# Optimization experiments

Hardware: AMD Instinct MI355X
Metric: run time of the kernel (lower is better)

## Reference

```python
import jax, jax.numpy as jnp
import numpy as np

B, L, C, H, W = 2, 3, 64, 32, 32
DI, N, DT_RANK, K = 128, 16, 4, 4  # d_inner=2*C, d_state, dt_rank=ceil(C/16), 4 scan dirs


def setup_inputs() -> dict:
    key = jax.random.key(0)
    ks = iter(jax.random.split(key, 48))
    nrm = lambda shape, s=0.02: jax.random.normal(next(ks), shape, jnp.float32) * s
    return {
        "image_sequence": jax.random.normal(next(ks), (B, L, C, H, W), jnp.float32),
        "difficult_zone": jax.random.normal(next(ks), (B, C, H, W), jnp.float32),
        "sigma": jax.random.uniform(next(ks), (B, C, H, W), jnp.float32),
        # LayerNorm2d applied to each frame
        "norm_g": jnp.ones((C,)), "norm_b": jnp.zeros((C,)),
        # ConvolutionalResBlock (in=3C -> out=C), GroupNorm(num_groups=1)
        "gn1_g": jnp.ones((3 * C,)), "gn1_b": jnp.zeros((3 * C,)),
        "conv1_w": nrm((C, 3 * C, 3, 3)), "conv1_b": jnp.zeros((C,)),
        "gn2_g": jnp.ones((C,)), "gn2_b": jnp.zeros((C,)),
        "conv2_w": nrm((C, C, 3, 3)), "conv2_b": jnp.zeros((C,)),
        "skip_w": nrm((C, 3 * C, 1, 1)), "skip_b": jnp.zeros((C,)),
        # VSSBlock pre-norms
        "ln1_g": jnp.ones((C,)), "ln1_b": jnp.zeros((C,)),
        "ln2_g": jnp.ones((C,)), "ln2_b": jnp.zeros((C,)),
        # SS2D
        "in_proj_w": nrm((2 * DI, C)),
        "dwconv_w": nrm((DI, 1, 3, 3)), "dwconv_b": jnp.zeros((DI,)),
        "x_proj_w": nrm((K, DT_RANK + 2 * N, DI)),
        "dt_proj_w": nrm((K, DI, DT_RANK), 0.1),
        "dt_proj_b": jnp.log(jnp.expm1(jnp.full((K, DI), 0.01, jnp.float32))),
        "A_logs": jnp.log(jnp.tile(jnp.arange(1, N + 1, dtype=jnp.float32), (K * DI, 1))),
        "Ds": jnp.ones((K * DI,)),
        "out_norm_g": jnp.ones((DI,)), "out_norm_b": jnp.zeros((DI,)),
        "out_proj_w": nrm((C, DI)),
        # Mlp (hidden = C)
        "fc1_w": nrm((C, C)), "fc1_b": jnp.zeros((C,)),
        "fc2_w": nrm((C, C)), "fc2_b": jnp.zeros((C,)),
    }


def _ln(x, g, b, eps=1e-5):  # layernorm over last axis
    m = x.mean(-1, keepdims=True)
    v = x.var(-1, keepdims=True)
    return (x - m) * jax.lax.rsqrt(v + eps) * g + b


def _ln2d(x, g, b, eps=1e-6):  # per-pixel channel layernorm, NCHW
    m = x.mean(1, keepdims=True)
    v = x.var(1, keepdims=True)
    return (x - m) * jax.lax.rsqrt(v + eps) * g[None, :, None, None] + b[None, :, None, None]


def _gn1(x, g, b, eps=1e-5):  # GroupNorm(num_groups=1), NCHW
    m = x.mean((1, 2, 3), keepdims=True)
    v = x.var((1, 2, 3), keepdims=True)
    return (x - m) * jax.lax.rsqrt(v + eps) * g[None, :, None, None] + b[None, :, None, None]


def _conv(x, w, b, pad):
    y = jax.lax.conv_general_dilated(x, w, (1, 1), [(pad, pad), (pad, pad)],
                                     dimension_numbers=("NCHW", "OIHW", "NCHW"))
    return y + b[None, :, None, None]


def _forward(image_sequence, difficult_zone, sigma, norm_g, norm_b, gn1_g, gn1_b,
             conv1_w, conv1_b, gn2_g, gn2_b, conv2_w, conv2_b, skip_w, skip_b,
             ln1_g, ln1_b, ln2_g, ln2_b, in_proj_w, dwconv_w, dwconv_b, x_proj_w,
             dt_proj_w, dt_proj_b, A_logs, Ds, out_norm_g, out_norm_b, out_proj_w,
             fc1_w, fc1_b, fc2_w, fc2_b):
    b, l, c, h, w = image_sequence.shape
    bl, L2 = b * l, h * w
    # fold frame loop into batch (identical math per frame in the torch loop)
    frames = _ln2d(image_sequence.reshape(bl, c, h, w), norm_g, norm_b)
    dz = jnp.broadcast_to(difficult_zone[:, None], (b, l, c, h, w)).reshape(bl, c, h, w)
    sg = jnp.broadcast_to(sigma[:, None], (b, l, c, h, w)).reshape(bl, c, h, w)
    x = jnp.concatenate([dz, frames, sg], axis=1)  # [bl, 3c, h, w]
    # channel compressor: pre-act conv res block
    hdn = _conv(jax.nn.silu(_gn1(x, gn1_g, gn1_b)), conv1_w, conv1_b, 1)
    hdn = _conv(jax.nn.silu(_gn1(hdn, gn2_g, gn2_b)), conv2_w, conv2_b, 1)
    x = hdn + _conv(x, skip_w, skip_b, 0)          # [bl, c, h, w]
    x = x.transpose(0, 2, 3, 1)                    # [bl, h, w, c]
    # --- VSSBlock (pre-norm): x = x + SS2D(LN(x)) ---
    xn = _ln(x, ln1_g, ln1_b)
    xz = xn @ in_proj_w.T                          # [bl,h,w,2*DI]
    xc, z = jnp.split(xz, 2, axis=-1)
    xc = xc.transpose(0, 3, 1, 2)                  # [bl, DI, h, w]
    xc = jax.lax.conv_general_dilated(xc, dwconv_w, (1, 1), [(1, 1), (1, 1)],
                                      dimension_numbers=("NCHW", "OIHW", "NCHW"),
                                      feature_group_count=DI) + dwconv_b[None, :, None, None]
    xc = jax.nn.silu(xc)
    # 4-direction scan inputs (HW, WH, and their reverses)
    xf = xc.reshape(bl, DI, L2)
    xt = xc.transpose(0, 1, 3, 2).reshape(bl, DI, L2)
    xs = jnp.stack([xf, xt], axis=1)
    xs = jnp.concatenate([xs, jnp.flip(xs, axis=-1)], axis=1)  # [bl, 4, DI, L2]
    x_dbl = jnp.einsum("bkdl,kcd->bkcl", xs, x_proj_w)
    dts, Bs, Cs = jnp.split(x_dbl, [DT_RANK, DT_RANK + N], axis=2)
    dts = jnp.einsum("bkrl,kdr->bkdl", dts, dt_proj_w) + dt_proj_b[None, :, :, None]
    dts = jax.nn.softplus(dts)                     # [bl, 4, DI, L2]
    A = -jnp.exp(A_logs).reshape(K, DI, N)
    dA = jnp.exp(dts[..., None] * A[None, :, :, None, :])            # [bl,4,DI,L2,N]
    dBu = dts[..., None] * Bs.transpose(0, 1, 3, 2)[:, :, None] * xs[..., None]
    a_t = dA.transpose(3, 0, 1, 2, 4)              # [L2, bl, 4, DI, N]
    bu_t = dBu.transpose(3, 0, 1, 2, 4)
    c_t = Cs.transpose(3, 0, 1, 2)                 # [L2, bl, 4, N]

    def step(hid, inp):
        a_i, bu_i, c_i = inp
        hid = a_i * hid + bu_i
        return hid, jnp.einsum("bkdn,bkn->bkd", hid, c_i)

    h0 = jnp.zeros((bl, K, DI, N), xs.dtype)
    _, ys = jax.lax.scan(step, h0, (a_t, bu_t, c_t))                 # [L2, bl, 4, DI]
    ys = ys.transpose(1, 2, 3, 0) + xs * Ds.reshape(K, DI)[None, :, :, None]
    inv = jnp.flip(ys[:, 2:4], axis=-1)
    y = (ys[:, 0] + inv[:, 0]
         + ys[:, 1].reshape(bl, DI, w, h).transpose(0, 1, 3, 2).reshape(bl, DI, L2)
         + inv[:, 1].reshape(bl, DI, w, h).transpose(0, 1, 3, 2).reshape(bl, DI, L2))
    y = _ln(y.transpose(0, 2, 1), out_norm_g, out_norm_b).reshape(bl, h, w, DI)
    y = y * jax.nn.silu(z)
    x = x + y @ out_proj_w.T
    # --- x = x + Mlp(LN(x)) ---
    xn = _ln(x, ln2_g, ln2_b)
    x = x + (jax.nn.gelu(xn @ fc1_w.T + fc1_b, approximate=False) @ fc2_w.T + fc2_b)
    return x.transpose(0, 3, 1, 2).reshape(b, l, c, h, w)


def reference(image_sequence, difficult_zone, sigma, norm_g, norm_b, gn1_g, gn1_b,
              conv1_w, conv1_b, gn2_g, gn2_b, conv2_w, conv2_b, skip_w, skip_b,
              ln1_g, ln1_b, ln2_g, ln2_b, in_proj_w, dwconv_w, dwconv_b, x_proj_w,
              dt_proj_w, dt_proj_b, A_logs, Ds, out_norm_g, out_norm_b, out_proj_w,
              fc1_w, fc1_b, fc2_w, fc2_b):
    return _forward(image_sequence, difficult_zone, sigma, norm_g, norm_b, gn1_g, gn1_b,
                    conv1_w, conv1_b, gn2_g, gn2_b, conv2_w, conv2_b, skip_w, skip_b,
                    ln1_g, ln1_b, ln2_g, ln2_b, in_proj_w, dwconv_w, dwconv_b, x_proj_w,
                    dt_proj_w, dt_proj_b, A_logs, Ds, out_norm_g, out_norm_b, out_proj_w,
                    fc1_w, fc1_b, fc2_w, fc2_b)
```

## Files before the change

kernel.cpp:

```cpp
#include <hip/hip_runtime.h>
#include <math.h>

#define BL    6
#define CCH   64
#define C3    192
#define L2    1024
#define DIC   128
#define NST   16
#define K4    4
#define PSTR  1088
#define NCH   32

#define LOG2E 1.44269504088896340736f
#define LN2C  0.69314718055994530942f

__device__ __forceinline__ float fexp(float x){ return __builtin_amdgcn_exp2f(x*LOG2E); }
__device__ __forceinline__ float fsilu(float x){ return x * __builtin_amdgcn_rcpf(1.f + fexp(-x)); }
__device__ __forceinline__ float fsoftplus(float x){
  if (x > 20.f) return x;
  return __builtin_amdgcn_logf(1.f + fexp(x)) * LN2C;
}
__device__ __forceinline__ float fgelu(float x){
  return 0.5f*x*(1.f + erff(x*0.70710678118654752440f));
}

__global__ __launch_bounds__(256) void k_ln2d(const float* __restrict__ img,
    const float* __restrict__ dz, const float* __restrict__ sg,
    const float* __restrict__ g, const float* __restrict__ b, float* __restrict__ x3c,
    float* __restrict__ psum1, float* __restrict__ psq1){
  __shared__ float ps[4][16], pq[4][16], gs[4], gq[4];
  int s = blockIdx.x >> 6;
  int pg = blockIdx.x & 63;
  int tid = threadIdx.x;
  int px = tid & 15; int cg = tid >> 4;
  int wv = tid >> 6; int lane = tid & 63;
  int p = pg*16 + px;
  int bsmp = s/3;
  const float* fr = img + (size_t)s*CCH*L2;
  float vals[4]; float sm=0.f, sq=0.f;
  #pragma unroll
  for (int j=0;j<4;++j){
    int c = cg*4 + j;
    float v = fr[c*L2 + p];
    vals[j]=v; sm+=v; sq+=v*v;
  }
  sm += __shfl_xor(sm,16,64); sq += __shfl_xor(sq,16,64);
  sm += __shfl_xor(sm,32,64); sq += __shfl_xor(sq,32,64);
  if (lane < 16){ ps[wv][lane]=sm; pq[wv][lane]=sq; }
  __syncthreads();
  sm = ps[0][px]+ps[1][px]+ps[2][px]+ps[3][px];
  sq = pq[0][px]+pq[1][px]+pq[2][px]+pq[3][px];
  float mean = sm*(1.f/CCH); float var = sq*(1.f/CCH)-mean*mean;
  float rs = rsqrtf(var + 1e-6f);
  float* o = x3c + (size_t)s*C3*L2;
  const float* dzp = dz + (size_t)bsmp*CCH*L2;
  const float* sgp = sg + (size_t)bsmp*CCH*L2;
  float gsm=0.f, gsq=0.f;
  #pragma unroll
  for (int j=0;j<4;++j){
    int c = cg*4+j;
    float dzv = dzp[c*L2+p];
    float nv  = (vals[j]-mean)*rs*g[c] + b[c];
    float sgv = sgp[c*L2+p];
    o[c*L2+p] = dzv;
    o[(CCH+c)*L2+p] = nv;
    o[(2*CCH+c)*L2+p] = sgv;
    gsm += dzv+nv+sgv; gsq += dzv*dzv+nv*nv+sgv*sgv;
  }
  for (int m=1;m<64;m<<=1){ gsm+=__shfl_xor(gsm,m,64); gsq+=__shfl_xor(gsq,m,64); }
  if (lane==0){ gs[wv]=gsm; gq[wv]=gsq; }
  __syncthreads();
  if (tid==0){
    psum1[blockIdx.x] = gs[0]+gs[1]+gs[2]+gs[3];
    psq1 [blockIdx.x] = gq[0]+gq[1]+gq[2]+gq[3];
  }
}

__global__ __launch_bounds__(256) void k_gnact_pad(const float* __restrict__ x,
    const float* __restrict__ psum, const float* __restrict__ psq,
    const float* __restrict__ g, const float* __restrict__ b,
    int ch, int parts, float inv_n, float eps, float* __restrict__ out){
  int bx = blockIdx.x;
  int s = bx / ch; int c = bx % ch;
  int tid = threadIdx.x;
  float sm=0.f, sq=0.f;
  for (int i=0;i<parts;++i){ sm += psum[s*parts+i]; sq += psq[s*parts+i]; }
  float mean = sm*inv_n;
  float var = sq*inv_n - mean*mean;
  float rs = rsqrtf(var + eps);
  float gc = g[c]*rs; float bc = b[c] - mean*rs*g[c];
  float4 v = *(const float4*)(x + (size_t)bx*1024 + tid*4);
  float4 o; o.x = fsilu(v.x*gc+bc); o.y = fsilu(v.y*gc+bc);
  o.z = fsilu(v.z*gc+bc); o.w = fsilu(v.w*gc+bc);
  float* pl = out + (size_t)bx*PSTR;
  *(float4*)(pl + 32 + tid*4) = o;
  float4 z4 = make_float4(0.f,0.f,0.f,0.f);
  if (tid < 8)  *(float4*)(pl + tid*4) = z4;
  else if (tid < 16) *(float4*)(pl + 1056 + (tid-8)*4) = z4;
}

__device__ __forceinline__ void conv_row_acc(float4& a0, float4& a1, float4 mid, float lf, float rt,
    const float* wp0, const float* wp1){
  float w0=wp0[0], w1=wp0[1], w2=wp0[2];
  a0.x = fmaf(w0,lf,   fmaf(w1,mid.x, fmaf(w2,mid.y, a0.x)));
  a0.y = fmaf(w0,mid.x,fmaf(w1,mid.y, fmaf(w2,mid.z, a0.y)));
  a0.z = fmaf(w0,mid.y,fmaf(w1,mid.z, fmaf(w2,mid.w, a0.z)));
  a0.w = fmaf(w0,mid.z,fmaf(w1,mid.w, fmaf(w2,rt,    a0.w)));
  float v0=wp1[0], v1=wp1[1], v2=wp1[2];
  a1.x = fmaf(v0,lf,   fmaf(v1,mid.x, fmaf(v2,mid.y, a1.x)));
  a1.y = fmaf(v0,mid.x,fmaf(v1,mid.y, fmaf(v2,mid.z, a1.y)));
  a1.z = fmaf(v0,mid.y,fmaf(v1,mid.z, fmaf(v2,mid.w, a1.z)));
  a1.w = fmaf(v0,mid.z,fmaf(v1,mid.w, fmaf(v2,rt,    a1.w)));
}

__device__ __forceinline__ void conv_ci_body(float4 m0, float4 m1, float4 m2, int q,
    const float* wp0, const float* wp1, float4& a0, float4& a1){
  float lf0=__shfl_up(m0.w,1,64), rt0=__shfl_down(m0.x,1,64);
  float lf1=__shfl_up(m1.w,1,64), rt1=__shfl_down(m1.x,1,64);
  float lf2=__shfl_up(m2.w,1,64), rt2=__shfl_down(m2.x,1,64);
  if (q==0){ lf0=0.f; lf1=0.f; lf2=0.f; }
  if (q==7){ rt0=0.f; rt1=0.f; rt2=0.f; }
  conv_row_acc(a0,a1,m0,lf0,rt0, wp0+0, wp1+0);
  conv_row_acc(a0,a1,m1,lf1,rt1, wp0+3, wp1+3);
  conv_row_acc(a0,a1,m2,lf2,rt2, wp0+6, wp1+6);
}

__global__ __launch_bounds__(256) void k_conv1_split(const float* __restrict__ xact,
    const float* __restrict__ w, float* __restrict__ part){
  int bx = blockIdx.x; int kk = bx&7; int cop=(bx>>3)&31; int s=bx>>8;
  int co0 = cop*2, co1 = co0+1;
  int tid = threadIdx.x; int row = tid>>3; int q = tid&7; int col0 = q*4;
  float4 a0 = make_float4(0.f,0.f,0.f,0.f);
  float4 a1 = make_float4(0.f,0.f,0.f,0.f);
  int ci0 = kk*24;
  const float* pl = xact + ((size_t)s*C3 + ci0)*PSTR + row*32 + col0;
  const float* wp0 = w + (size_t)(co0*C3 + ci0)*9;
  const float* wp1 = w + (size_t)(co1*C3 + ci0)*9;
  float4 m0 = *(const float4*)(pl);
  float4 m1 = *(const float4*)(pl+32);
  float4 m2 = *(const float4*)(pl+64);
  #pragma unroll 2
  for (int i=0;i<24;++i){
    const float* pn = pl + (i<23 ? PSTR : 0);
    float4 n0 = *(const float4*)(pn);
    float4 n1 = *(const float4*)(pn+32);
    float4 n2 = *(const float4*)(pn+64);
    conv_ci_body(m0,m1,m2,q, wp0, wp1, a0, a1);
    wp0 += 9; wp1 += 9; pl = pn; m0=n0; m1=n1; m2=n2;
  }
  float* pp = part + (size_t)kk*(BL*CCH*L2) + ((size_t)s*CCH+co0)*L2 + row*32+col0;
  *(float4*)pp = a0;
  *(float4*)(pp+L2) = a1;
}

__global__ __launch_bounds__(256) void k_reduce1(const float* __restrict__ part,
    const float* __restrict__ bias, float* __restrict__ h1,
    float* __restrict__ psum2, float* __restrict__ psq2){
  int co = blockIdx.x & 63; int s = blockIdx.x >> 6;
  size_t ofs = ((size_t)s*CCH+co)*L2 + threadIdx.x*4;
  const size_t stride = (size_t)BL*CCH*L2;
  float4 acc = *(const float4*)(part + ofs);
  #pragma unroll
  for (int kk=1;kk<8;++kk){
    float4 r = *(const float4*)(part + (size_t)kk*stride + ofs);
    acc.x += r.x; acc.y += r.y; acc.z += r.z; acc.w += r.w;
  }
  float bv = bias[co];
  acc.x += bv; acc.y += bv; acc.z += bv; acc.w += bv;
  *(float4*)(h1 + ofs) = acc;
  float sm = acc.x+acc.y+acc.z+acc.w;
  float sq = acc.x*acc.x+acc.y*acc.y+acc.z*acc.z+acc.w*acc.w;
  for (int m=1;m<64;m<<=1){ sm+=__shfl_xor(sm,m,64); sq+=__shfl_xor(sq,m,64); }
  __shared__ float s_sm[4], s_sq[4];
  int wv = threadIdx.x>>6;
  if ((threadIdx.x&63)==0){ s_sm[wv]=sm; s_sq[wv]=sq; }
  __syncthreads();
  if (threadIdx.x==0){
    psum2[blockIdx.x] = s_sm[0]+s_sm[1]+s_sm[2]+s_sm[3];
    psq2 [blockIdx.x] = s_sq[0]+s_sq[1]+s_sq[2]+s_sq[3];
  }
}

__global__ __launch_bounds__(256) void k_conv2_split(const float* __restrict__ xact2,
    const float* __restrict__ x3c, const float* __restrict__ w2,
    const float* __restrict__ wsk, float* __restrict__ part){
  int t = blockIdx.x; int role = t % 3; t /= 3;
  int cop = t & 31; int s = t >> 5;
  int co0 = cop*2, co1 = co0+1;
  int tid = threadIdx.x; int row = tid>>3; int q = tid&7; int col0 = q*4;
  int p = row*32+col0;
  float4 a0 = make_float4(0.f,0.f,0.f,0.f);
  float4 a1 = make_float4(0.f,0.f,0.f,0.f);
  if (role < 2){
    int ci0 = role*32;
    const float* pl = xact2 + ((size_t)s*CCH + ci0)*PSTR + row*32 + col0;
    const float* wp0 = w2 + (size_t)(co0*CCH + ci0)*9;
    const float* wp1 = w2 + (size_t)(co1*CCH + ci0)*9;
    float4 m0 = *(const float4*)(pl);
    float4 m1 = *(const float4*)(pl+32);
    float4 m2 = *(const float4*)(pl+64);
    #pragma unroll 2
    for (int i=0;i<32;++i){
      const float* pn = pl + (i<31 ? PSTR : 0);
      float4 n0 = *(const float4*)(pn);
      float4 n1 = *(const float4*)(pn+32);
      float4 n2 = *(const float4*)(pn+64);
      conv_ci_body(m0,m1,m2,q, wp0, wp1, a0, a1);
      wp0 += 9; wp1 += 9; pl = pn; m0=n0; m1=n1; m2=n2;
    }
  } else {
    const float* x3 = x3c + (size_t)s*C3*L2 + p;
    #pragma unroll 4
    for (int ci=0; ci<C3; ++ci){
      float4 v = *(const float4*)(x3 + (size_t)ci*L2);
      float ws0 = wsk[co0*C3+ci], ws1 = wsk[co1*C3+ci];
      a0.x = fmaf(ws0,v.x,a0.x); a0.y = fmaf(ws0,v.y,a0.y); a0.z = fmaf(ws0,v.z,a0.z); a0.w = fmaf(ws0,v.w,a0.w);
      a1.x = fmaf(ws1,v.x,a1.x); a1.y = fmaf(ws1,v.y,a1.y); a1.z = fmaf(ws1,v.z,a1.z); a1.w = fmaf(ws1,v.w,a1.w);
    }
  }
  float* pp = part + (size_t)role*(BL*CCH*L2) + ((size_t)s*CCH+co0)*L2 + p;
  *(float4*)pp = a0;
  *(float4*)(pp+L2) = a1;
}

__global__ __launch_bounds__(256) void k_red2_ln1_inproj(const float* __restrict__ part,
    const float* __restrict__ b2, const float* __restrict__ bsk,
    const float* __restrict__ g, const float* __restrict__ b,
    const float* __restrict__ W,
    float* __restrict__ x_cmaj, float* __restrict__ xc, float* __restrict__ z_t){
  __shared__ float xn_s[64*65];
  int bx = blockIdx.x; int oq = bx & 3; int pg = (bx>>2)&15; int s = bx>>6;
  int p0 = pg*64;
  int tid = threadIdx.x;
  const size_t stride = (size_t)BL*CCH*L2;
  #pragma unroll
  for (int kq=0;kq<4;++kq){
    int f = kq*256 + tid;
    int co = f >> 4; int px4 = (f & 15)*4;
    size_t ofs = ((size_t)s*CCH+co)*L2 + p0 + px4;
    float4 r0 = *(const float4*)(part + ofs);
    float4 r1 = *(const float4*)(part + stride + ofs);
    float4 r2 = *(const float4*)(part + 2*stride + ofs);
    float bv = b2[co]+bsk[co];
    float4 o;
    o.x = r0.x+r1.x+r2.x+bv;
    o.y = r0.y+r1.y+r2.y+bv;
    o.z = r0.z+r1.z+r2.z+bv;
    o.w = r0.w+r1.w+r2.w+bv;
    if (oq == 0) *(float4*)(x_cmaj + ofs) = o;
    xn_s[(px4+0)*65 + co] = o.x;
    xn_s[(px4+1)*65 + co] = o.y;
    xn_s[(px4+2)*65 + co] = o.z;
    xn_s[(px4+3)*65 + co] = o.w;
  }
  __syncthreads();
  {
    int wv = __builtin_amdgcn_readfirstlane(tid>>6); int lane = tid&63;
    for (int j=0;j<16;++j){
      int pl = wv*16 + j;
      float v = xn_s[pl*65 + lane];
      float sm = v, sq = v*v;
      for (int m=1;m<64;m<<=1){ sm += __shfl_xor(sm,m,64); sq += __shfl_xor(sq,m,64); }
      float mean = sm*(1.f/64.f); float var = sq*(1.f/64.f) - mean*mean;
      float rs = rsqrtf(var + 1e-5f);
      xn_s[pl*65 + lane] = (v-mean)*rs*g[lane] + b[lane];
    }
  }
  __syncthreads();
  int px_l = tid & 63;
  int og = __builtin_amdgcn_readfirstlane(tid >> 6);
  int o0 = oq*64 + og*16;
  float acc[16];
  #pragma unroll
  for (int oi=0;oi<16;++oi) acc[oi]=0.f;
  for (int c=0;c<64;++c){
    float xv = xn_s[px_l*65 + c];
    #pragma unroll
    for (int oi=0;oi<16;++oi) acc[oi] = fmaf(W[(o0+oi)*64 + c], xv, acc[oi]);
  }
  int p = p0 + px_l;
  if (oq < 2){
    #pragma unroll
    for (int oi=0;oi<16;++oi) xc[((size_t)s*DIC + o0 + oi)*L2 + p] = acc[oi];
  } else {
    #pragma unroll
    for (int oi=0;oi<16;++oi) z_t[((size_t)s*DIC + (o0-128) + oi)*L2 + p] = acc[oi];
  }
}

__global__ __launch_bounds__(256) void k_xproj_dt(const float* __restrict__ xc,
    const float* __restrict__ dww, const float* __restrict__ dwb,
    const float* __restrict__ W,
    float* __restrict__ dtr, float* __restrict__ Bp, float* __restrict__ Cp,
    float* __restrict__ u_t){
  __shared__ float smem[128*68];
  int bx = blockIdx.x; int pg = bx & 15; int sk = bx >> 4;
  int k = sk & 3; int s = sk >> 2;
  int tid = threadIdx.x;
  for (int i = tid; i < 128*16; i += 256){
    int dr = i>>4; int j4 = (i&15)*4;
    int rw = j4>>5; int col0 = j4 & 31;
    int gr = pg*2 + rw;
    int q = i&7;
    const float* xr = xc + ((size_t)s*DIC+dr)*L2;
    const float* wp = dww + dr*9;
    float bv = dwb[dr];
    float4 acc = make_float4(bv,bv,bv,bv);
    #pragma unroll
    for (int dy=-1;dy<=1;++dy){
      int r = gr+dy;
      float4 mid = make_float4(0.f,0.f,0.f,0.f);
      if (0<=r && r<32) mid = *(const float4*)(xr + r*32 + col0);
      float lf = __shfl_up(mid.w,1,64); if(q==0) lf=0.f;
      float rt = __shfl_down(mid.x,1,64); if(q==7) rt=0.f;
      float w0=wp[(dy+1)*3], w1=wp[(dy+1)*3+1], w2=wp[(dy+1)*3+2];
      acc.x = fmaf(w0,lf,   fmaf(w1,mid.x, fmaf(w2,mid.y, acc.x)));
      acc.y = fmaf(w0,mid.x,fmaf(w1,mid.y, fmaf(w2,mid.z, acc.y)));
      acc.z = fmaf(w0,mid.y,fmaf(w1,mid.z, fmaf(w2,mid.w, acc.z)));
      acc.w = fmaf(w0,mid.z,fmaf(w1,mid.w, fmaf(w2,rt,    acc.w)));
    }
    acc.x = fsilu(acc.x); acc.y = fsilu(acc.y); acc.z = fsilu(acc.z); acc.w = fsilu(acc.w);
    *(float4*)&smem[dr*68 + j4] = acc;
  }
  __syncthreads();
  if (k == 0){
    float* ub = u_t + ((size_t)(s*L2) + pg*64)*DIC;
    for (int i = tid; i < 64*128; i += 256){
      int px2 = i>>7; int dd = i&127;
      ub[(size_t)px2*DIC + dd] = smem[dd*68 + px2];
    }
  }
  int px = tid & 63;
  int cgrp = __builtin_amdgcn_readfirstlane(tid >> 6);
  int c0 = cgrp*9;
  const float* wb = W + (size_t)(k*36 + c0)*DIC;
  float acc[9];
  #pragma unroll
  for (int ci=0;ci<9;++ci) acc[ci]=0.f;
  for (int d=0; d<DIC; ++d){
    float xv = smem[d*68 + px];
    #pragma unroll
    for (int ci=0;ci<9;++ci) acc[ci] = fmaf(wb[ci*DIC+d], xv, acc[ci]);
  }
  __syncthreads();
  #pragma unroll
  for (int ci=0;ci<9;++ci) smem[(c0+ci)*68 + px] = acc[ci];
  __syncthreads();
  {
    int pp = tid >> 2; int r = tid & 3;
    dtr[((size_t)sk*L2 + pg*64 + pp)*4 + r] = smem[r*68 + pp];
  }
  float* Bb = Bp + ((size_t)sk*L2 + pg*64)*NST;
  float* Cb = Cp + ((size_t)sk*L2 + pg*64)*NST;
  for (int i = tid; i < 1024; i += 256){
    int pp = i>>4; int n = i&15;
    Bb[pp*NST + n] = smem[(4+n)*68 + pp];
    Cb[pp*NST + n] = smem[(20+n)*68 + pp];
  }
}

__device__ __forceinline__ int scan_pix32(int ch, int j, int k){
  if (k==0) return ch*32 + j;
  if (k==1) return j*32 + ch;
  if (k==2) return 1023 - (ch*32 + j);
  return 1023 - (j*32 + ch);
}

struct StepB { float4 dt4; float uv; float4 B0,B1,B2,B3; };
__device__ __forceinline__ StepB loadB(const float* dr, const float* ub, const float* Bb, int p){
  StepB r;
  r.dt4 = *(const float4*)(dr + (size_t)p*4);
  r.uv = ub[(size_t)p*DIC];
  const float* bp = Bb + p*NST;
  r.B0 = *(const float4*)bp; r.B1 = *(const float4*)(bp+4);
  r.B2 = *(const float4*)(bp+8); r.B3 = *(const float4*)(bp+12);
  return r;
}
__device__ __forceinline__ float dt_eval(float4 w4, float bb, float4 d4){
  return fsoftplus(fmaf(w4.x,d4.x,fmaf(w4.y,d4.y,fmaf(w4.z,d4.z,fmaf(w4.w,d4.w,bb)))));
}

__global__ __launch_bounds__(256,2) void k_scan_part3(const float* __restrict__ dtr,
    const float* __restrict__ dtw, const float* __restrict__ dtb,
    const float* __restrict__ u_t, const float* __restrict__ Bp,
    const float* __restrict__ A_logs, float* __restrict__ hend, float* __restrict__ Ssum){
  int bx = blockIdx.x; int chp = bx & 15; int sk = bx >> 4;
  int k = sk & 3; int s = sk >> 2;
  int tid = threadIdx.x; int d = tid & 127; int ch = chp*2 + (tid>>7);
  float aco[16];
  {
    const float* ab = A_logs + (size_t)(k*DIC+d)*NST;
    #pragma unroll
    for (int n=0;n<16;++n) aco[n] = -LOG2E * fexp(ab[n]);
  }
  float4 w4 = *(const float4*)(dtw + (size_t)(k*DIC+d)*4);
  float bb = dtb[k*DIC+d];
  float h[16]; float Sacc = 0.f;
  #pragma unroll
  for (int n=0;n<16;++n) h[n]=0.f;
  const float* dr = dtr + (size_t)sk*L2*4;
  const float* ub = u_t + (size_t)s*L2*DIC + d;
  const float* Bb = Bp + (size_t)sk*L2*NST;
  StepB cur = loadB(dr, ub, Bb, scan_pix32(ch, 0, k));
  #pragma unroll 4
  for (int j=0;j<32;++j){
    StepB nxt;
    if (j < 31) nxt = loadB(dr, ub, Bb, scan_pix32(ch, j+1, k));
    float dtv = dt_eval(w4, bb, cur.dt4);
    Sacc += dtv;
    float tv = dtv*cur.uv;
    #define PSTEP(NI, BV) { float a_ = __builtin_amdgcn_exp2f(dtv*aco[NI]); \
      h[NI] = fmaf(a_, h[NI], tv*(BV)); }
    PSTEP(0,cur.B0.x) PSTEP(1,cur.B0.y) PSTEP(2,cur.B0.z) PSTEP(3,cur.B0.w)
    PSTEP(4,cur.B1.x) PSTEP(5,cur.B1.y) PSTEP(6,cur.B1.z) PSTEP(7,cur.B1.w)
    PSTEP(8,cur.B2.x) PSTEP(9,cur.B2.y) PSTEP(10,cur.B2.z) PSTEP(11,cur.B2.w)
    PSTEP(12,cur.B3.x) PSTEP(13,cur.B3.y) PSTEP(14,cur.B3.z) PSTEP(15,cur.B3.w)
    #undef PSTEP
    cur = nxt;
  }
  size_t base = ((size_t)(sk*NCH + ch)*DIC + d)*NST;
  #pragma unroll
  for (int q4=0;q4<4;++q4)
    *(float4*)(hend + base + q4*4)  = make_float4(h[q4*4],h[q4*4+1],h[q4*4+2],h[q4*4+3]);
  Ssum[(size_t)(sk*NCH + ch)*DIC + d] = Sacc;
}

__global__ __launch_bounds__(256) void k_scan_fix3(const float* __restrict__ hend,
    const float* __restrict__ Ssum, const float* __restrict__ A_logs,
    float* __restrict__ Hin){
  int t = blockIdx.x*256 + threadIdx.x;
  int n = t & 15; int d = (t>>4) & 127; int sk = t >> 11; int k = sk & 3;
  float aco = -LOG2E * fexp(A_logs[(size_t)(k*DIC+d)*NST + n]);
  float H = 0.f;
  #pragma unroll 8
  for (int ch=0; ch<NCH; ++ch){
    size_t sidx = (size_t)(sk*NCH + ch)*DIC + d;
    float pa = __builtin_amdgcn_exp2f(aco * Ssum[sidx]);
    float he = hend[sidx*NST + n];
    Hin[sidx*NST + n] = H;
    H = fmaf(pa, H, he);
  }
}

__global__ __launch_bounds__(256,2) void k_scan_y3(const float* __restrict__ dtr,
    const float* __restrict__ dtw, const float* __restrict__ dtb,
    const float* __restrict__ u_t, const float* __restrict__ Bp, const float* __restrict__ Cp,
    const float* __restrict__ A_logs, const float* __restrict__ Ds,
    const float* __restrict__ Hin, float* __restrict__ ys_t){
  int bx = blockIdx.x; int chp = bx & 15; int sk = bx >> 4;
  int k = sk & 3; int s = sk >> 2;
  int tid = threadIdx.x; int d = tid & 127; int ch = chp*2 + (tid>>7);
  float aco[16];
  {
    const float* ab = A_logs + (size_t)(k*DIC+d)*NST;
    #pragma unroll
    for (int n=0;n<16;++n) aco[n] = -LOG2E * fexp(ab[n]);
  }
  float4 w4 = *(const float4*)(dtw + (size_t)(k*DIC+d)*4);
  float bb = dtb[k*DIC+d];
  float Dv = Ds[k*DIC+d];
  float h[16];
  size_t hbase = ((size_t)(sk*NCH + ch)*DIC + d)*NST;
  #pragma unroll
  for (int q4=0;q4<4;++q4){
    float4 hv = *(const float4*)(Hin + hbase + q4*4);
    h[q4*4]=hv.x; h[q4*4+1]=hv.y; h[q4*4+2]=hv.z; h[q4*4+3]=hv.w;
  }
  const float* dr = dtr + (size_t)sk*L2*4;
  const float* ub = u_t + (size_t)s*L2*DIC + d;
  const float* Bb = Bp + (size_t)sk*L2*NST;
  const float* Cb = Cp + (size_t)sk*L2*NST;
  float* yb = ys_t + (size_t)sk*L2*DIC + d;
  int pcur = scan_pix32(ch, 0, k);
  StepB cur = loadB(dr, ub, Bb, pcur);
  float4 Cc0 = *(const float4*)(Cb + pcur*NST);
  float4 Cc1 = *(const float4*)(Cb + pcur*NST + 4);
  float4 Cc2 = *(const float4*)(Cb + pcur*NST + 8);
  float4 Cc3 = *(const float4*)(Cb + pcur*NST + 12);
  #pragma unroll 4
  for (int j=0;j<32;++j){
    StepB nxt; float4 Cn0, Cn1, Cn2, Cn3; int pn = pcur;
    if (j < 31){
      pn = scan_pix32(ch, j+1, k);
      nxt = loadB(dr, ub, Bb, pn);
      Cn0 = *(const float4*)(Cb + pn*NST);
      Cn1 = *(const float4*)(Cb + pn*NST + 4);
      Cn2 = *(const float4*)(Cb + pn*NST + 8);
      Cn3 = *(const float4*)(Cb + pn*NST + 12);
    }
    float dtv = dt_eval(w4, bb, cur.dt4);
    float tv = dtv*cur.uv;
    float y0=0.f, y1=0.f, y2=0.f, y3=0.f;
    #define YSTEP(NI, BV, CV, YA) { float a_ = __builtin_amdgcn_exp2f(dtv*aco[NI]); \
      h[NI] = fmaf(a_, h[NI], tv*(BV)); YA = fmaf(h[NI], (CV), YA); }
    YSTEP(0,cur.B0.x,Cc0.x,y0) YSTEP(1,cur.B0.y,Cc0.y,y1) YSTEP(2,cur.B0.z,Cc0.z,y2) YSTEP(3,cur.B0.w,Cc0.w,y3)
    YSTEP(4,cur.B1.x,Cc1.x,y0) YSTEP(5,cur.B1.y,Cc1.y,y1) YSTEP(6,cur.B1.z,Cc1.z,y2) YSTEP(7,cur.B1.w,Cc1.w,y3)
    YSTEP(8,cur.B2.x,Cc2.x,y0) YSTEP(9,cur.B2.y,Cc2.y,y1) YSTEP(10,cur.B2.z,Cc2.z,y2) YSTEP(11,cur.B2.w,Cc2.w,y3)
    YSTEP(12,cur.B3.x,Cc3.x,y0) YSTEP(13,cur.B3.y,Cc3.y,y1) YSTEP(14,cur.B3.z,Cc3.z,y2) YSTEP(15,cur.B3.w,Cc3.w,y3)
    #undef YSTEP
    yb[(size_t)pcur*DIC] = fmaf(cur.uv, Dv, (y0+y1)+(y2+y3));
    cur = nxt; Cc0 = Cn0; Cc1 = Cn1; Cc2 = Cn2; Cc3 = Cn3; pcur = pn;
  }
}

__global__ __launch_bounds__(256) void k_tail(const float* __restrict__ ys_t,
    const float* __restrict__ z_t, const float* __restrict__ ong, const float* __restrict__ onb,
    const float* __restrict__ Wop, const float* __restrict__ x_cmaj,
    const float* __restrict__ g2, const float* __restrict__ b2n,
    const float* __restrict__ w1, const float* __restrict__ b1,
    const float* __restrict__ w2, const float* __restrict__ b2,
    float* __restrict__ out){
  __shared__ float yt[128*17];
  __shared__ float xvt[64*17];
  __shared__ float ts[64*17];
  int s = blockIdx.x >> 6; int pg = blockIdx.x & 63;
  int tid = threadIdx.x;
  {
    int wv = __builtin_amdgcn_readfirstlane(tid>>6); int lane = tid&63;
    int d0 = lane, d1 = lane+64;
    for (int i=0;i<4;++i){
      int px = i*4 + wv; int p = pg*16 + px;
      const float* yb = ys_t + ((size_t)(s*4)*L2 + p)*DIC;
      float ya = yb[d0] + yb[(size_t)L2*DIC + d0] + yb[(size_t)2*L2*DIC + d0] + yb[(size_t)3*L2*DIC + d0];
      float yc = yb[d1] + yb[(size_t)L2*DIC + d1] + yb[(size_t)2*L2*DIC + d1] + yb[(size_t)3*L2*DIC + d1];
      float sm = ya+yc, sq = ya*ya+yc*yc;
      for (int m=1;m<64;m<<=1){ sm+=__shfl_xor(sm,m,64); sq+=__shfl_xor(sq,m,64); }
      float mean = sm*(1.f/128.f); float var = sq*(1.f/128.f)-mean*mean;
      float rs = rsqrtf(var + 1e-5f);
      float yn0 = (ya-mean)*rs*ong[d0] + onb[d0];
      float yn1 = (yc-mean)*rs*ong[d1] + onb[d1];
      float zv0 = z_t[((size_t)s*DIC+d0)*L2 + p];
      float zv1 = z_t[((size_t)s*DIC+d1)*L2 + p];
      yt[d0*17 + px] = yn0 * fsilu(zv0);
      yt[d1*17 + px] = yn1 * fsilu(zv1);
    }
  }
  __syncthreads();
  {
    int px = tid & 15; int cgp = tid >> 4;
    int c0 = cgp*4;
    float a0=0.f,a1=0.f,a2=0.f,a3=0.f;
    for (int d=0; d<DIC; ++d){
      float yv = yt[d*17 + px];
      a0 = fmaf(Wop[(c0+0)*DIC + d], yv, a0);
      a1 = fmaf(Wop[(c0+1)*DIC + d], yv, a1);
      a2 = fmaf(Wop[(c0+2)*DIC + d], yv, a2);
      a3 = fmaf(Wop[(c0+3)*DIC + d], yv, a3);
    }
    int p = pg*16 + px;
    size_t base = ((size_t)s*CCH + c0)*L2 + p;
    xvt[(c0+0)*17 + px] = x_cmaj[base]      + a0;
    xvt[(c0+1)*17 + px] = x_cmaj[base+L2]   + a1;
    xvt[(c0+2)*17 + px] = x_cmaj[base+2*L2] + a2;
    xvt[(c0+3)*17 + px] = x_cmaj[base+3*L2] + a3;
  }
  __syncthreads();
  int px = tid & 15; int cgp = tid >> 4;
  float sm=0.f, sq=0.f;
  for (int c=0;c<64;++c){ float v = xvt[c*17+px]; sm+=v; sq+=v*v; }
  float mean = sm*(1.f/64.f);
  float rs = rsqrtf(sq*(1.f/64.f) - mean*mean + 1e-5f);
  int o0 = cgp*4;
  float t[4];
  #pragma unroll
  for (int oi=0;oi<4;++oi) t[oi] = b1[o0+oi];
  for (int c=0;c<64;++c){
    float xn = (xvt[c*17+px]-mean)*rs*g2[c] + b2n[c];
    #pragma unroll
    for (int oi=0;oi<4;++oi) t[oi] = fmaf(xn, w1[(o0+oi)*64 + c], t[oi]);
  }
  #pragma unroll
  for (int oi=0;oi<4;++oi) ts[(o0+oi)*17 + px] = fgelu(t[oi]);
  __syncthreads();
  int c0 = cgp*4;
  float acc[4];
  #pragma unroll
  for (int ci=0;ci<4;++ci) acc[ci] = xvt[(c0+ci)*17+px] + b2[c0+ci];
  for (int o=0;o<64;++o){
    float tv = ts[o*17+px];
    #pragma unroll
    for (int ci=0;ci<4;++ci) acc[ci] = fmaf(tv, w2[(c0+ci)*64 + o], acc[ci]);
  }
  int p = pg*16 + px;
  #pragma unroll
  for (int ci=0;ci<4;++ci) out[((size_t)s*CCH + c0+ci)*L2 + p] = acc[ci];
}

extern "C" void kernel_launch(void* const* d_in, const int* in_sizes, int n_in,
                              void* d_out, int out_size, void* d_ws, size_t ws_size,
                              hipStream_t stream){
  (void)in_sizes; (void)n_in; (void)out_size; (void)ws_size;
  const float* img      = (const float*)d_in[0];
  const float* dz       = (const float*)d_in[1];
  const float* sg       = (const float*)d_in[2];
  const float* norm_g   = (const float*)d_in[3];
  const float* norm_b   = (const float*)d_in[4];
  const float* gn1_g    = (const float*)d_in[5];
  const float* gn1_b    = (const float*)d_in[6];
  const float* conv1_w  = (const float*)d_in[7];
  const float* conv1_b  = (const float*)d_in[8];
  const float* gn2_g    = (const float*)d_in[9];
  const float* gn2_b    = (const float*)d_in[10];
  const float* conv2_w  = (const float*)d_in[11];
  const float* conv2_b  = (const float*)d_in[12];
  const float* skip_w   = (const float*)d_in[13];
  const float* skip_b   = (const float*)d_in[14];
  const float* ln1_g    = (const float*)d_in[15];
  const float* ln1_b    = (const float*)d_in[16];
  const float* ln2_g    = (const float*)d_in[17];
  const float* ln2_b    = (const float*)d_in[18];
  const float* in_proj_w= (const float*)d_in[19];
  const float* dwconv_w = (const float*)d_in[20];
  const float* dwconv_b = (const float*)d_in[21];
  const float* x_proj_w = (const float*)d_in[22];
  const float* dt_proj_w= (const float*)d_in[23];
  const float* dt_proj_b= (const float*)d_in[24];
  const float* A_logs   = (const float*)d_in[25];
  const float* Ds       = (const float*)d_in[26];
  const float* out_norm_g = (const float*)d_in[27];
  const float* out_norm_b = (const float*)d_in[28];
  const float* out_proj_w = (const float*)d_in[29];
  const float* fc1_w    = (const float*)d_in[30];
  const float* fc1_b    = (const float*)d_in[31];
  const float* fc2_w    = (const float*)d_in[32];
  const float* fc2_b    = (const float*)d_in[33];

  float* ws = (float*)d_ws;
  float* x3c    = ws;
  float* xact1  = x3c    + 1179648;
  float* h1     = xact1  + 1253376;
  float* xact2  = h1     + 393216;
  float* xpslot = xact2  + 417792;
  float* x_cmaj = xpslot + 393216;
  float* z_t    = x_cmaj + 393216;
  float* xc     = z_t    + 786432;
  float* cpslot = xc     + 786432;
  float* hole   = cpslot + 786432;
  float* scanbuf= hole   + 884736;
  float* ys_t   = scanbuf+ 3145728;
  float* statsb = ys_t   + 3145728;
  float* psum1  = statsb;
  float* psq1   = statsb + 384;
  float* psum2  = statsb + 768;
  float* psq2   = statsb + 1152;
  float* part1  = scanbuf;
  float* part2  = ys_t;
  float* hend   = x3c;
  float* u_t    = h1;
  float* Bp     = xpslot;
  float* Cp     = cpslot;
  float* dtr    = hole;
  float* Ssum   = hole + 98304;
  float* Hin    = scanbuf;

  k_ln2d<<<384, 256, 0, stream>>>(img, dz, sg, norm_g, norm_b, x3c, psum1, psq1);
  k_gnact_pad<<<6*C3, 256, 0, stream>>>(x3c, psum1, psq1, gn1_g, gn1_b, C3, 64,
                                        1.f/(C3*L2), 1e-5f, xact1);
  k_conv1_split<<<1536, 256, 0, stream>>>(xact1, conv1_w, part1);
  k_reduce1<<<384, 256, 0, stream>>>(part1, conv1_b, h1, psum2, psq2);
  k_gnact_pad<<<6*CCH, 256, 0, stream>>>(h1, psum2, psq2, gn2_g, gn2_b, CCH, 64,
                                         1.f/(CCH*L2), 1e-5f, xact2);
  k_conv2_split<<<576, 256, 0, stream>>>(xact2, x3c, conv2_w, skip_w, part2);
  k_red2_ln1_inproj<<<384, 256, 0, stream>>>(part2, conv2_b, skip_b, ln1_g, ln1_b, in_proj_w,
                                             x_cmaj, xc, z_t);
  k_xproj_dt<<<384, 256, 0, stream>>>(xc, dwconv_w, dwconv_b, x_proj_w, dtr, Bp, Cp, u_t);
  k_scan_part3<<<384, 256, 0, stream>>>(dtr, dt_proj_w, dt_proj_b, u_t, Bp, A_logs, hend, Ssum);
  k_scan_fix3<<<192, 256, 0, stream>>>(hend, Ssum, A_logs, Hin);
  k_scan_y3<<<384, 256, 0, stream>>>(dtr, dt_proj_w, dt_proj_b, u_t, Bp, Cp, A_logs, Ds, Hin, ys_t);
  k_tail<<<384, 256, 0, stream>>>(ys_t, z_t, out_norm_g, out_norm_b, out_proj_w, x_cmaj,
                                  ln2_g, ln2_b, fc1_w, fc1_b, fc2_w, fc2_b, (float*)d_out);
}
```

Baseline: 305.3 us.

## Split conv2, in_proj and scan kernels across more blocks for parallelism

Conv2 and skip work is split six ways along input channels instead of three. The reduction now sums six partials, and in_proj uses eight output groups instead of four. Both scan kernels split the 16 state dims across thread pairs, launching one chunk per block with twice the blocks and combining y via a lane shuffle. This adds CU occupancy on a small problem at the cost of more partial-buffer traffic, duplicated loads of dt and u, and a larger part2 buffer that must fit its aliased slot.

```diff
diff --git a/kernel.cpp b/kernel.cpp
--- a/kernel.cpp
+++ b/kernel.cpp
@@ -184,15 +184,15 @@
 __global__ __launch_bounds__(256) void k_conv2_split(const float* __restrict__ xact2,
     const float* __restrict__ x3c, const float* __restrict__ w2,
     const float* __restrict__ wsk, float* __restrict__ part){
-  int t = blockIdx.x; int role = t % 3; t /= 3;
+  int t = blockIdx.x; int role = t % 6; t /= 6;
   int cop = t & 31; int s = t >> 5;
   int co0 = cop*2, co1 = co0+1;
   int tid = threadIdx.x; int row = tid>>3; int q = tid&7; int col0 = q*4;
   int p = row*32+col0;
   float4 a0 = make_float4(0.f,0.f,0.f,0.f);
   float4 a1 = make_float4(0.f,0.f,0.f,0.f);
-  if (role < 2){
-    int ci0 = role*32;
+  if (role < 4){
+    int ci0 = role*16;
     const float* pl = xact2 + ((size_t)s*CCH + ci0)*PSTR + row*32 + col0;
     const float* wp0 = w2 + (size_t)(co0*CCH + ci0)*9;
     const float* wp1 = w2 + (size_t)(co1*CCH + ci0)*9;
@@ -200,8 +200,8 @@
     float4 m1 = *(const float4*)(pl+32);
     float4 m2 = *(const float4*)(pl+64);
     #pragma unroll 2
-    for (int i=0;i<32;++i){
-      const float* pn = pl + (i<31 ? PSTR : 0);
+    for (int i=0;i<16;++i){
+      const float* pn = pl + (i<15 ? PSTR : 0);
       float4 n0 = *(const float4*)(pn);
       float4 n1 = *(const float4*)(pn+32);
       float4 n2 = *(const float4*)(pn+64);
@@ -209,11 +209,14 @@
       wp0 += 9; wp1 += 9; pl = pn; m0=n0; m1=n1; m2=n2;
     }
   } else {
-    const float* x3 = x3c + (size_t)s*C3*L2 + p;
+    int ci0 = (role-4)*96;
+    const float* x3 = x3c + ((size_t)s*C3 + ci0)*L2 + p;
+    const float* w0p = wsk + co0*C3 + ci0;
+    const float* w1p = wsk + co1*C3 + ci0;
     #pragma unroll 4
-    for (int ci=0; ci<C3; ++ci){
+    for (int ci=0; ci<96; ++ci){
       float4 v = *(const float4*)(x3 + (size_t)ci*L2);
-      float ws0 = wsk[co0*C3+ci], ws1 = wsk[co1*C3+ci];
+      float ws0 = w0p[ci], ws1 = w1p[ci];
       a0.x = fmaf(ws0,v.x,a0.x); a0.y = fmaf(ws0,v.y,a0.y); a0.z = fmaf(ws0,v.z,a0.z); a0.w = fmaf(ws0,v.w,a0.w);
       a1.x = fmaf(ws1,v.x,a1.x); a1.y = fmaf(ws1,v.y,a1.y); a1.z = fmaf(ws1,v.z,a1.z); a1.w = fmaf(ws1,v.w,a1.w);
     }
@@ -229,7 +232,7 @@
     const float* __restrict__ W,
     float* __restrict__ x_cmaj, float* __restrict__ xc, float* __restrict__ z_t){
   __shared__ float xn_s[64*65];
-  int bx = blockIdx.x; int oq = bx & 3; int pg = (bx>>2)&15; int s = bx>>6;
+  int bx = blockIdx.x; int oq = bx & 7; int pg = (bx>>3)&15; int s = bx>>7;
   int p0 = pg*64;
   int tid = threadIdx.x;
   const size_t stride = (size_t)BL*CCH*L2;
@@ -241,12 +244,15 @@
     float4 r0 = *(const float4*)(part + ofs);
     float4 r1 = *(const float4*)(part + stride + ofs);
     float4 r2 = *(const float4*)(part + 2*stride + ofs);
+    float4 r3 = *(const float4*)(part + 3*stride + ofs);
+    float4 r4 = *(const float4*)(part + 4*stride + ofs);
+    float4 r5 = *(const float4*)(part + 5*stride + ofs);
     float bv = b2[co]+bsk[co];
     float4 o;
-    o.x = r0.x+r1.x+r2.x+bv;
-    o.y = r0.y+r1.y+r2.y+bv;
-    o.z = r0.z+r1.z+r2.z+bv;
-    o.w = r0.w+r1.w+r2.w+bv;
+    o.x = ((r0.x+r1.x)+(r2.x+r3.x))+(r4.x+r5.x)+bv;
+    o.y = ((r0.y+r1.y)+(r2.y+r3.y))+(r4.y+r5.y)+bv;
+    o.z = ((r0.z+r1.z)+(r2.z+r3.z))+(r4.z+r5.z)+bv;
+    o.w = ((r0.w+r1.w)+(r2.w+r3.w))+(r4.w+r5.w)+bv;
     if (oq == 0) *(float4*)(x_cmaj + ofs) = o;
     xn_s[(px4+0)*65 + co] = o.x;
     xn_s[(px4+1)*65 + co] = o.y;
@@ -269,22 +275,22 @@
   __syncthreads();
   int px_l = tid & 63;
   int og = __builtin_amdgcn_readfirstlane(tid >> 6);
-  int o0 = oq*64 + og*16;
-  float acc[16];
-  #pragma unroll
-  for (int oi=0;oi<16;++oi) acc[oi]=0.f;
+  int o0 = oq*32 + og*8;
+  float acc[8];
+  #pragma unroll
+  for (int oi=0;oi<8;++oi) acc[oi]=0.f;
   for (int c=0;c<64;++c){
     float xv = xn_s[px_l*65 + c];
     #pragma unroll
-    for (int oi=0;oi<16;++oi) acc[oi] = fmaf(W[(o0+oi)*64 + c], xv, acc[oi]);
+    for (int oi=0;oi<8;++oi) acc[oi] = fmaf(W[(o0+oi)*64 + c], xv, acc[oi]);
   }
   int p = p0 + px_l;
-  if (oq < 2){
-    #pragma unroll
-    for (int oi=0;oi<16;++oi) xc[((size_t)s*DIC + o0 + oi)*L2 + p] = acc[oi];
+  if (oq < 4){
+    #pragma unroll
+    for (int oi=0;oi<8;++oi) xc[((size_t)s*DIC + o0 + oi)*L2 + p] = acc[oi];
   } else {
     #pragma unroll
-    for (int oi=0;oi<16;++oi) z_t[((size_t)s*DIC + (o0-128) + oi)*L2 + p] = acc[oi];
+    for (int oi=0;oi<8;++oi) z_t[((size_t)s*DIC + (o0-128) + oi)*L2 + p] = acc[oi];
   }
 }
 
@@ -366,46 +372,45 @@
   return 1023 - (j*32 + ch);
 }
 
-struct StepB { float4 dt4; float uv; float4 B0,B1,B2,B3; };
-__device__ __forceinline__ StepB loadB(const float* dr, const float* ub, const float* Bb, int p){
-  StepB r;
+struct StepH { float4 dt4; float uv; float4 B0,B1; };
+__device__ __forceinline__ StepH loadH(const float* dr, const float* ub, const float* Bb, int p){
+  StepH r;
   r.dt4 = *(const float4*)(dr + (size_t)p*4);
   r.uv = ub[(size_t)p*DIC];
   const float* bp = Bb + p*NST;
   r.B0 = *(const float4*)bp; r.B1 = *(const float4*)(bp+4);
-  r.B2 = *(const float4*)(bp+8); r.B3 = *(const float4*)(bp+12);
   return r;
 }
 __device__ __forceinline__ float dt_eval(float4 w4, float bb, float4 d4){
   return fsoftplus(fmaf(w4.x,d4.x,fmaf(w4.y,d4.y,fmaf(w4.z,d4.z,fmaf(w4.w,d4.w,bb)))));
 }
 
-__global__ __launch_bounds__(256,2) void k_scan_part3(const float* __restrict__ dtr,
+__global__ __launch_bounds__(256,4) void k_scan_part3(const float* __restrict__ dtr,
     const float* __restrict__ dtw, const float* __restrict__ dtb,
     const float* __restrict__ u_t, const float* __restrict__ Bp,
     const float* __restrict__ A_logs, float* __restrict__ hend, float* __restrict__ Ssum){
-  int bx = blockIdx.x; int chp = bx & 15; int sk = bx >> 4;
+  int bx = blockIdx.x; int ch = bx & 31; int sk = bx >> 5;
   int k = sk & 3; int s = sk >> 2;
-  int tid = threadIdx.x; int d = tid & 127; int ch = chp*2 + (tid>>7);
-  float aco[16];
+  int tid = threadIdx.x; int d = tid >> 1; int nh = tid & 1;
+  float aco[8];
   {
-    const float* ab = A_logs + (size_t)(k*DIC+d)*NST;
-    #pragma unroll
-    for (int n=0;n<16;++n) aco[n] = -LOG2E * fexp(ab[n]);
+    const float* ab = A_logs + (size_t)(k*DIC+d)*NST + nh*8;
+    #pragma unroll
+    for (int n=0;n<8;++n) aco[n] = -LOG2E * fexp(ab[n]);
   }
   float4 w4 = *(const float4*)(dtw + (size_t)(k*DIC+d)*4);
   float bb = dtb[k*DIC+d];
-  float h[16]; float Sacc = 0.f;
-  #pragma unroll
-  for (int n=0;n<16;++n) h[n]=0.f;
+  float h[8]; float Sacc = 0.f;
+  #pragma unroll
+  for (int n=0;n<8;++n) h[n]=0.f;
   const float* dr = dtr + (size_t)sk*L2*4;
   const float* ub = u_t + (size_t)s*L2*DIC + d;
-  const float* Bb = Bp + (size_t)sk*L2*NST;
-  StepB cur = loadB(dr, ub, Bb, scan_pix32(ch, 0, k));
+  const float* Bb = Bp + (size_t)sk*L2*NST + nh*8;
+  StepH cur = loadH(dr, ub, Bb, scan_pix32(ch, 0, k));
   #pragma unroll 4
   for (int j=0;j<32;++j){
-    StepB nxt;
-    if (j < 31) nxt = loadB(dr, ub, Bb, scan_pix32(ch, j+1, k));
+    StepH nxt;
+    if (j < 31) nxt = loadH(dr, ub, Bb, scan_pix32(ch, j+1, k));
     float dtv = dt_eval(w4, bb, cur.dt4);
     Sacc += dtv;
     float tv = dtv*cur.uv;
@@ -413,16 +418,13 @@
       h[NI] = fmaf(a_, h[NI], tv*(BV)); }
     PSTEP(0,cur.B0.x) PSTEP(1,cur.B0.y) PSTEP(2,cur.B0.z) PSTEP(3,cur.B0.w)
     PSTEP(4,cur.B1.x) PSTEP(5,cur.B1.y) PSTEP(6,cur.B1.z) PSTEP(7,cur.B1.w)
-    PSTEP(8,cur.B2.x) PSTEP(9,cur.B2.y) PSTEP(10,cur.B2.z) PSTEP(11,cur.B2.w)
-    PSTEP(12,cur.B3.x) PSTEP(13,cur.B3.y) PSTEP(14,cur.B3.z) PSTEP(15,cur.B3.w)
     #undef PSTEP
     cur = nxt;
   }
-  size_t base = ((size_t)(sk*NCH + ch)*DIC + d)*NST;
-  #pragma unroll
-  for (int q4=0;q4<4;++q4)
-    *(float4*)(hend + base + q4*4)  = make_float4(h[q4*4],h[q4*4+1],h[q4*4+2],h[q4*4+3]);
-  Ssum[(size_t)(sk*NCH + ch)*DIC + d] = Sacc;
+  size_t base = ((size_t)(sk*NCH + ch)*DIC + d)*NST + nh*8;
+  *(float4*)(hend + base)     = make_float4(h[0],h[1],h[2],h[3]);
+  *(float4*)(hend + base + 4) = make_float4(h[4],h[5],h[6],h[7]);
+  if (nh == 0) Ssum[(size_t)(sk*NCH + ch)*DIC + d] = Sacc;
 }
 
 __global__ __launch_bounds__(256) void k_scan_fix3(const float* __restrict__ hend,
@@ -442,51 +444,48 @@
   }
 }
 
-__global__ __launch_bounds__(256,2) void k_scan_y3(const float* __restrict__ dtr,
+__global__ __launch_bounds__(256,4) void k_scan_y3(const float* __restrict__ dtr,
     const float* __restrict__ dtw, const float* __restrict__ dtb,
     const float* __restrict__ u_t, const float* __restrict__ Bp, const float* __restrict__ Cp,
     const float* __restrict__ A_logs, const float* __restrict__ Ds,
     const float* __restrict__ Hin, float* __restrict__ ys_t){
-  int bx = blockIdx.x; int chp = bx & 15; int sk = bx >> 4;
+  int bx = blockIdx.x; int ch = bx & 31; int sk = bx >> 5;
   int k = sk & 3; int s = sk >> 2;
-  int tid = threadIdx.x; int d = tid & 127; int ch = chp*2 + (tid>>7);
-  float aco[16];
+  int tid = threadIdx.x; int d = tid >> 1; int nh = tid & 1;
+  float aco[8];
   {
-    const float* ab = A_logs + (size_t)(k*DIC+d)*NST;
-    #pragma unroll
-    for (int n=0;n<16;++n) aco[n] = -LOG2E * fexp(ab[n]);
+    const float* ab = A_logs + (size_t)(k*DIC+d)*NST + nh*8;
+    #pragma unroll
+    for (int n=0;n<8;++n) aco[n] = -LOG2E * fexp(ab[n]);
   }
   float4 w4 = *(const float4*)(dtw + (size_t)(k*DIC+d)*4);
   float bb = dtb[k*DIC+d];
   float Dv = Ds[k*DIC+d];
-  float h[16];
-  size_t hbase = ((size_t)(sk*NCH + ch)*DIC + d)*NST;
-  #pragma unroll
-  for (int q4=0;q4<4;++q4){
-    float4 hv = *(const float4*)(Hin + hbase + q4*4);
-    h[q4*4]=hv.x; h[q4*4+1]=hv.y; h[q4*4+2]=hv.z; h[q4*4+3]=hv.w;
+  float h[8];
+  size_t hbase = ((size_t)(sk*NCH + ch)*DIC + d)*NST + nh*8;
+  {
+    float4 h0 = *(const float4*)(Hin + hbase);
+    float4 h1 = *(const float4*)(Hin + hbase + 4);
+    h[0]=h0.x; h[1]=h0.y; h[2]=h0.z; h[3]=h0.w;
+    h[4]=h1.x; h[5]=h1.y; h[6]=h1.z; h[7]=h1.w;
   }
   const float* dr = dtr + (size_t)sk*L2*4;
   const float* ub = u_t + (size_t)s*L2*DIC + d;
-  const float* Bb = Bp + (size_t)sk*L2*NST;
-  const float* Cb = Cp + (size_t)sk*L2*NST;
+  const float* Bb = Bp + (size_t)sk*L2*NST + nh*8;
+  const float* Cb = Cp + (size_t)sk*L2*NST + nh*8;
   float* yb = ys_t + (size_t)sk*L2*DIC + d;
   int pcur = scan_pix32(ch, 0, k);
-  StepB cur = loadB(dr, ub, Bb, pcur);
+  StepH cur = loadH(dr, ub, Bb, pcur);
   float4 Cc0 = *(const float4*)(Cb + pcur*NST);
   float4 Cc1 = *(const float4*)(Cb + pcur*NST + 4);
-  float4 Cc2 = *(const float4*)(Cb + pcur*NST + 8);
-  float4 Cc3 = *(const float4*)(Cb + pcur*NST + 12);
   #pragma unroll 4
   for (int j=0;j<32;++j){
-    StepB nxt; float4 Cn0, Cn1, Cn2, Cn3; int pn = pcur;
+    StepH nxt; float4 Cn0, Cn1; int pn = pcur;
     if (j < 31){
       pn = scan_pix32(ch, j+1, k);
-      nxt = loadB(dr, ub, Bb, pn);
+      nxt = loadH(dr, ub, Bb, pn);
       Cn0 = *(const float4*)(Cb + pn*NST);
       Cn1 = *(const float4*)(Cb + pn*NST + 4);
-      Cn2 = *(const float4*)(Cb + pn*NST + 8);
-      Cn3 = *(const float4*)(Cb + pn*NST + 12);
     }
     float dtv = dt_eval(w4, bb, cur.dt4);
     float tv = dtv*cur.uv;
@@ -495,11 +494,11 @@
       h[NI] = fmaf(a_, h[NI], tv*(BV)); YA = fmaf(h[NI], (CV), YA); }
     YSTEP(0,cur.B0.x,Cc0.x,y0) YSTEP(1,cur.B0.y,Cc0.y,y1) YSTEP(2,cur.B0.z,Cc0.z,y2) YSTEP(3,cur.B0.w,Cc0.w,y3)
     YSTEP(4,cur.B1.x,Cc1.x,y0) YSTEP(5,cur.B1.y,Cc1.y,y1) YSTEP(6,cur.B1.z,Cc1.z,y2) YSTEP(7,cur.B1.w,Cc1.w,y3)
-    YSTEP(8,cur.B2.x,Cc2.x,y0) YSTEP(9,cur.B2.y,Cc2.y,y1) YSTEP(10,cur.B2.z,Cc2.z,y2) YSTEP(11,cur.B2.w,Cc2.w,y3)
-    YSTEP(12,cur.B3.x,Cc3.x,y0) YSTEP(13,cur.B3.y,Cc3.y,y1) YSTEP(14,cur.B3.z,Cc3.z,y2) YSTEP(15,cur.B3.w,Cc3.w,y3)
     #undef YSTEP
-    yb[(size_t)pcur*DIC] = fmaf(cur.uv, Dv, (y0+y1)+(y2+y3));
-    cur = nxt; Cc0 = Cn0; Cc1 = Cn1; Cc2 = Cn2; Cc3 = Cn3; pcur = pn;
+    float py = (y0+y1)+(y2+y3);
+    float tot = py + __shfl_xor(py, 1, 64);
+    if (nh == 0) yb[(size_t)pcur*DIC] = fmaf(cur.uv, Dv, tot);
+    cur = nxt; Cc0 = Cn0; Cc1 = Cn1; pcur = pn;
   }
 }
 
@@ -660,13 +659,13 @@
   k_reduce1<<<384, 256, 0, stream>>>(part1, conv1_b, h1, psum2, psq2);
   k_gnact_pad<<<6*CCH, 256, 0, stream>>>(h1, psum2, psq2, gn2_g, gn2_b, CCH, 64,
                                          1.f/(CCH*L2), 1e-5f, xact2);
-  k_conv2_split<<<576, 256, 0, stream>>>(xact2, x3c, conv2_w, skip_w, part2);
-  k_red2_ln1_inproj<<<384, 256, 0, stream>>>(part2, conv2_b, skip_b, ln1_g, ln1_b, in_proj_w,
+  k_conv2_split<<<1152, 256, 0, stream>>>(xact2, x3c, conv2_w, skip_w, part2);
+  k_red2_ln1_inproj<<<768, 256, 0, stream>>>(part2, conv2_b, skip_b, ln1_g, ln1_b, in_proj_w,
                                              x_cmaj, xc, z_t);
   k_xproj_dt<<<384, 256, 0, stream>>>(xc, dwconv_w, dwconv_b, x_proj_w, dtr, Bp, Cp, u_t);
-  k_scan_part3<<<384, 256, 0, stream>>>(dtr, dt_proj_w, dt_proj_b, u_t, Bp, A_logs, hend, Ssum);
+  k_scan_part3<<<768, 256, 0, stream>>>(dtr, dt_proj_w, dt_proj_b, u_t, Bp, A_logs, hend, Ssum);
   k_scan_fix3<<<192, 256, 0, stream>>>(hend, Ssum, A_logs, Hin);
-  k_scan_y3<<<384, 256, 0, stream>>>(dtr, dt_proj_w, dt_proj_b, u_t, Bp, Cp, A_logs, Ds, Hin, ys_t);
+  k_scan_y3<<<768, 256, 0, stream>>>(dtr, dt_proj_w, dt_proj_b, u_t, Bp, Cp, A_logs, Ds, Hin, ys_t);
   k_tail<<<384, 256, 0, stream>>>(ys_t, z_t, out_norm_g, out_norm_b, out_proj_w, x_cmaj,
                                   ln2_g, ln2_b, fc1_w, fc1_b, fc2_w, fc2_b, (float*)d_out);
 }
```

Result: faster. 291.2 us (-4.6%).
